# Performance work log

Measured on AMD Instinct MI355X. Metric: run time of the kernel, lower is better.

## Reference

```python
import jax, jax.numpy as jnp
import numpy as np

N_POINTS = 500000   # collocation points
N_TERMS = 64        # library terms
N_OUT = 4           # number of outputs / equations


def setup_inputs() -> dict:
    key = jax.random.key(0)
    k1, k2 = jax.random.split(key)
    thetas = jax.random.normal(k1, (N_POINTS, N_TERMS), dtype=jnp.float32)
    # n_out time derivatives packed as columns of a single [N, n_out] array
    time_derivs = jax.random.normal(k2, (N_POINTS, N_OUT), dtype=jnp.float32)
    return {"thetas": thetas, "time_derivs": time_derivs}


def reference(thetas, time_derivs):
    # sparsity masks are all-True at init, so apply_mask is identity and all
    # n_out least-squares problems share the same (full) library matrix.
    sparse_theta = thetas  # [N, n_terms]
    xtx = thetas.T @ thetas              # [n_terms, n_terms] (shared Gram)
    xty = thetas.T @ time_derivs         # [n_terms, n_out]
    # torch.inverse(X^T X) @ (X^T y), batched over outputs as columns
    coeffs = jnp.linalg.inv(xtx) @ xty   # [n_terms, n_out]
    return (sparse_theta, coeffs)
```

## Files before the change

### kernel.cpp

```cpp
#include <hip/hip_runtime.h>

#define N_ROWS   500000
#define N_TERMS  64
#define N_OUT    4
#define CHUNK_R  32
#define NCHUNK   (N_ROWS / CHUNK_R)
#define NB       512
#define WAVES_PB 8
#define WAVES_TOTAL (NB * WAVES_PB)
#define PART_STRIDE (N_TERMS * N_TERMS + N_TERMS * N_OUT)
#define CHUNKS   8
#define PER_CHUNK (NB / CHUNKS)
#define JACOBI_ITERS 20

typedef float f32x4   __attribute__((ext_vector_type(4)));
typedef short bf16x8  __attribute__((ext_vector_type(8)));

__device__ inline unsigned short f32_bf16(float f) {
  unsigned int u = __builtin_bit_cast(unsigned int, f);
  u += 0x7fffu + ((u >> 16) & 1u);
  return (unsigned short)(u >> 16);
}

__device__ inline bf16x8 frag_col(const float* __restrict__ Tf, int cswz, int k0) {
  bf16x8 r;
#pragma unroll
  for (int j = 0; j < 8; ++j)
    r[j] = (short)f32_bf16(Tf[(k0 + j) * 64 + cswz]);
  return r;
}

__global__ __launch_bounds__(512, 4) void k1_gram(const float* __restrict__ th,
                                                  const float* __restrict__ td,
                                                  float* __restrict__ out_copy,
                                                  float* __restrict__ part) {
  __shared__ float4 W4[WAVES_PB * 544];

  const int tid  = threadIdx.x;
  const int wv   = tid >> 6;
  const int lane = tid & 63;
  const int g    = lane >> 4;
  const int l15  = lane & 15;
  const int kg   = g * 8;
  const int szf  = (g & 1) << 4;

  float4* Wt = W4 + wv * 544;
  float4* Wy = Wt + 512;
  const float* Tf = (const float*)Wt;

  f32x4 c00 = {0.f,0.f,0.f,0.f}, c01 = c00, c02 = c00, c03 = c00;
  f32x4 c11 = c00, c12 = c00, c13 = c00, c22 = c00, c23 = c00, c33 = c00;
  float accY[4] = {0.f, 0.f, 0.f, 0.f};

  const float4* th4 = (const float4*)th;
  const float4* td4 = (const float4*)td;
  float4* out4 = (float4*)out_copy;

  for (int ch = blockIdx.x * WAVES_PB + wv; ch < NCHUNK; ch += WAVES_TOTAL) {
    const size_t r0 = (size_t)ch * CHUNK_R;
    const float4* src = th4 + r0 * 16;
    float4*       dst = out4 + r0 * 16;

    float4 cur[8];
#pragma unroll
    for (int j = 0; j < 8; ++j) cur[j] = src[j * 64 + lane];
    float4 yv = make_float4(0.f, 0.f, 0.f, 0.f);
    if (lane < 32) yv = td4[r0 + lane];

#pragma unroll
    for (int j = 0; j < 8; ++j) {
      dst[j * 64 + lane] = cur[j];
      const int fi  = j * 64 + lane;
      const int swz = ((fi >> 7) & 1) << 2;
      Wt[(fi & ~15) | ((fi & 15) ^ swz)] = cur[j];
    }
    if (lane < 32) Wy[lane] = yv;

    bf16x8 fr[4];
#pragma unroll
    for (int i = 0; i < 4; ++i)
      fr[i] = frag_col(Tf, (16 * i + l15) ^ szf, kg);

    c00 = __builtin_amdgcn_mfma_f32_16x16x32_bf16(fr[0], fr[0], c00, 0, 0, 0);
    c01 = __builtin_amdgcn_mfma_f32_16x16x32_bf16(fr[0], fr[1], c01, 0, 0, 0);
    c02 = __builtin_amdgcn_mfma_f32_16x16x32_bf16(fr[0], fr[2], c02, 0, 0, 0);
    c03 = __builtin_amdgcn_mfma_f32_16x16x32_bf16(fr[0], fr[3], c03, 0, 0, 0);
    c11 = __builtin_amdgcn_mfma_f32_16x16x32_bf16(fr[1], fr[1], c11, 0, 0, 0);
    c12 = __builtin_amdgcn_mfma_f32_16x16x32_bf16(fr[1], fr[2], c12, 0, 0, 0);
    c13 = __builtin_amdgcn_mfma_f32_16x16x32_bf16(fr[1], fr[3], c13, 0, 0, 0);
    c22 = __builtin_amdgcn_mfma_f32_16x16x32_bf16(fr[2], fr[2], c22, 0, 0, 0);
    c23 = __builtin_amdgcn_mfma_f32_16x16x32_bf16(fr[2], fr[3], c23, 0, 0, 0);
    c33 = __builtin_amdgcn_mfma_f32_16x16x32_bf16(fr[3], fr[3], c33, 0, 0, 0);

#pragma unroll
    for (int r = 0; r < CHUNK_R; ++r) {
      const int sz = ((r >> 3) & 1) << 4;
      const float  tv = Tf[r * 64 + (lane ^ sz)];
      const float4 yr = Wy[r];
      accY[0] += tv * yr.x;
      accY[1] += tv * yr.y;
      accY[2] += tv * yr.z;
      accY[3] += tv * yr.w;
    }
  }

  __syncthreads();
  float* red  = (float*)W4;
  float* yred = red + 64 * 65;

  for (int w = 0; w < WAVES_PB; ++w) {
    if (wv == w) {
      const bool first = (w == 0);
#define WR_TILE(A, B, C)                                                    \
  {                                                                         \
    _Pragma("unroll") for (int r = 0; r < 4; ++r) {                         \
      const int e = (16 * (A) + 4 * g + r) * 65 + 16 * (B) + l15;           \
      if (first) red[e] = (C)[r]; else red[e] += (C)[r];                    \
    }                                                                       \
  }
#define WR_TILE_T(A, B, C)                                                  \
  {                                                                         \
    _Pragma("unroll") for (int r = 0; r < 4; ++r) {                         \
      const int e = (16 * (B) + l15) * 65 + 16 * (A) + 4 * g + r;           \
      if (first) red[e] = (C)[r]; else red[e] += (C)[r];                    \
    }                                                                       \
  }
      WR_TILE(0, 0, c00);
      WR_TILE(0, 1, c01); WR_TILE_T(0, 1, c01);
      WR_TILE(0, 2, c02); WR_TILE_T(0, 2, c02);
      WR_TILE(0, 3, c03); WR_TILE_T(0, 3, c03);
      WR_TILE(1, 1, c11);
      WR_TILE(1, 2, c12); WR_TILE_T(1, 2, c12);
      WR_TILE(1, 3, c13); WR_TILE_T(1, 3, c13);
      WR_TILE(2, 2, c22);
      WR_TILE(2, 3, c23); WR_TILE_T(2, 3, c23);
      WR_TILE(3, 3, c33);
#undef WR_TILE
#undef WR_TILE_T
#pragma unroll
      for (int o = 0; o < 4; ++o) {
        const int e = lane * 4 + o;
        if (first) yred[e] = accY[o]; else yred[e] += accY[o];
      }
    }
    __syncthreads();
  }

  float* p = part + blockIdx.x * PART_STRIDE;
#pragma unroll
  for (int s = 0; s < 8; ++s) {
    const int e = s * 512 + tid;
    p[e] = red[(e >> 6) * 65 + (e & 63)];
  }
  if (tid < 256) p[4096 + tid] = yred[tid];
}

__global__ __launch_bounds__(256) void k2a_reduce(const float* __restrict__ part,
                                                  float* __restrict__ mid) {
  const int eblk = blockIdx.x % 17;
  const int bch  = blockIdx.x / 17;
  const int e = eblk * 256 + threadIdx.x;
  if (e >= PART_STRIDE) return;
  const float* base = part + (size_t)bch * PER_CHUNK * PART_STRIDE + e;
  float s = 0.f;
  for (int i = 0; i < PER_CHUNK; ++i) s += base[i * PART_STRIDE];
  mid[bch * PART_STRIDE + e] = s;
}

__global__ __launch_bounds__(256) void k3_solve(const float* __restrict__ mid,
                                                float* __restrict__ coef_out) {
  __shared__ float A[64 * 65];
  __shared__ float bX[64 * 4];
  __shared__ float X0[64 * 4];
  __shared__ float X1[64 * 4];
  const int tid = threadIdx.x;

#pragma unroll
  for (int s = 0; s < 17; ++s) {
    const int e = s * 256 + tid;
    if (e < PART_STRIDE) {
      float v = 0.f;
#pragma unroll
      for (int c = 0; c < CHUNKS; ++c) v += mid[c * PART_STRIDE + e];
      if (e < 4096) A[(e >> 6) * 65 + (e & 63)] = v;
      else          bX[e - 4096] = v;
    }
  }
  __syncthreads();

  const int i = tid >> 2;
  const int c = tid & 3;

  float arow[64];
#pragma unroll
  for (int j = 0; j < 64; ++j) arow[j] = A[i * 65 + j];

  const float dinv = 1.0f / A[i * 65 + i];
  const float b = bX[i * 4 + c];

  float x0 = b * dinv;
  X0[tid] = x0;
  __syncthreads();

  float xlast = x0;
  for (int it = 0; it < JACOBI_ITERS; ++it) {
    const float* Xr = (it & 1) ? X1 : X0;
    float*       Xw = (it & 1) ? X0 : X1;
    float s0 = 0.f, s1 = 0.f, s2 = 0.f, s3 = 0.f;
#pragma unroll
    for (int j = 0; j < 64; j += 4) {
      s0 += arow[j]     * Xr[(j)     * 4 + c];
      s1 += arow[j + 1] * Xr[(j + 1) * 4 + c];
      s2 += arow[j + 2] * Xr[(j + 2) * 4 + c];
      s3 += arow[j + 3] * Xr[(j + 3) * 4 + c];
    }
    const float s = (s0 + s1) + (s2 + s3);
    xlast = xlast + (b - s) * dinv;
    Xw[tid] = xlast;
    __syncthreads();
  }

  coef_out[tid] = xlast;
}

extern "C" void kernel_launch(void* const* d_in, const int* in_sizes, int n_in,
                              void* d_out, int out_size, void* d_ws, size_t ws_size,
                              hipStream_t stream) {
  const float* th = (const float*)d_in[0];
  const float* td = (const float*)d_in[1];
  float* out = (float*)d_out;
  float* ws  = (float*)d_ws;

  float* part = ws;
  float* mid  = ws + (size_t)NB * PART_STRIDE;

  hipLaunchKernelGGL(k1_gram, dim3(NB), dim3(512), 0, stream, th, td, out, part);
  hipLaunchKernelGGL(k2a_reduce, dim3(17 * CHUNKS), dim3(256), 0, stream, part, mid);
  hipLaunchKernelGGL(k3_solve, dim3(1), dim3(256), 0, stream, mid,
                     out + (size_t)N_ROWS * N_TERMS);
}
```

Before: 76.08 us.

## Split Gram kernel into copy waves and prefetching MFMA Gram waves

Result: slower. 159.2 us (+109.3%).

```diff
diff --git a/kernel.cpp b/kernel.cpp
--- a/kernel.cpp
+++ b/kernel.cpp
@@ -6,8 +6,8 @@
 #define CHUNK_R  32
 #define NCHUNK   (N_ROWS / CHUNK_R)
 #define NB       512
-#define WAVES_PB 8
-#define WAVES_TOTAL (NB * WAVES_PB)
+#define GRAM_WAVES_TOTAL (NB * 4)
+#define F4_TOTAL (N_ROWS * (N_TERMS / 4))
 #define PART_STRIDE (N_TERMS * N_TERMS + N_TERMS * N_OUT)
 #define CHUNKS   8
 #define PER_CHUNK (NB / CHUNKS)
@@ -34,7 +34,7 @@
                                                   const float* __restrict__ td,
                                                   float* __restrict__ out_copy,
                                                   float* __restrict__ part) {
-  __shared__ float4 W4[WAVES_PB * 544];
+  __shared__ float4 W4[4 * 544];
 
   const int tid  = threadIdx.x;
   const int wv   = tid >> 6;
@@ -44,63 +44,98 @@
   const int kg   = g * 8;
   const int szf  = (g & 1) << 4;
 
-  float4* Wt = W4 + wv * 544;
-  float4* Wy = Wt + 512;
-  const float* Tf = (const float*)Wt;
+  const float4* th4 = (const float4*)th;
+  const float4* td4 = (const float4*)td;
+  float4* out4 = (float4*)out_copy;
 
   f32x4 c00 = {0.f,0.f,0.f,0.f}, c01 = c00, c02 = c00, c03 = c00;
   f32x4 c11 = c00, c12 = c00, c13 = c00, c22 = c00, c23 = c00, c33 = c00;
   float accY[4] = {0.f, 0.f, 0.f, 0.f};
 
-  const float4* th4 = (const float4*)th;
-  const float4* td4 = (const float4*)td;
-  float4* out4 = (float4*)out_copy;
-
-  for (int ch = blockIdx.x * WAVES_PB + wv; ch < NCHUNK; ch += WAVES_TOTAL) {
-    const size_t r0 = (size_t)ch * CHUNK_R;
-    const float4* src = th4 + r0 * 16;
-    float4*       dst = out4 + r0 * 16;
-
-    float4 cur[8];
-#pragma unroll
-    for (int j = 0; j < 8; ++j) cur[j] = src[j * 64 + lane];
-    float4 yv = make_float4(0.f, 0.f, 0.f, 0.f);
-    if (lane < 32) yv = td4[r0 + lane];
-
-#pragma unroll
-    for (int j = 0; j < 8; ++j) {
-      dst[j * 64 + lane] = cur[j];
-      const int fi  = j * 64 + lane;
-      const int swz = ((fi >> 7) & 1) << 2;
-      Wt[(fi & ~15) | ((fi & 15) ^ swz)] = cur[j];
-    }
-    if (lane < 32) Wy[lane] = yv;
-
-    bf16x8 fr[4];
-#pragma unroll
-    for (int i = 0; i < 4; ++i)
-      fr[i] = frag_col(Tf, (16 * i + l15) ^ szf, kg);
-
-    c00 = __builtin_amdgcn_mfma_f32_16x16x32_bf16(fr[0], fr[0], c00, 0, 0, 0);
-    c01 = __builtin_amdgcn_mfma_f32_16x16x32_bf16(fr[0], fr[1], c01, 0, 0, 0);
-    c02 = __builtin_amdgcn_mfma_f32_16x16x32_bf16(fr[0], fr[2], c02, 0, 0, 0);
-    c03 = __builtin_amdgcn_mfma_f32_16x16x32_bf16(fr[0], fr[3], c03, 0, 0, 0);
-    c11 = __builtin_amdgcn_mfma_f32_16x16x32_bf16(fr[1], fr[1], c11, 0, 0, 0);
-    c12 = __builtin_amdgcn_mfma_f32_16x16x32_bf16(fr[1], fr[2], c12, 0, 0, 0);
-    c13 = __builtin_amdgcn_mfma_f32_16x16x32_bf16(fr[1], fr[3], c13, 0, 0, 0);
-    c22 = __builtin_amdgcn_mfma_f32_16x16x32_bf16(fr[2], fr[2], c22, 0, 0, 0);
-    c23 = __builtin_amdgcn_mfma_f32_16x16x32_bf16(fr[2], fr[3], c23, 0, 0, 0);
-    c33 = __builtin_amdgcn_mfma_f32_16x16x32_bf16(fr[3], fr[3], c33, 0, 0, 0);
-
-#pragma unroll
-    for (int r = 0; r < CHUNK_R; ++r) {
-      const int sz = ((r >> 3) & 1) << 4;
-      const float  tv = Tf[r * 64 + (lane ^ sz)];
-      const float4 yr = Wy[r];
-      accY[0] += tv * yr.x;
-      accY[1] += tv * yr.y;
-      accY[2] += tv * yr.z;
-      accY[3] += tv * yr.w;
+  if (wv >= 4) {
+    const int cwid = blockIdx.x * 4 + (wv - 4);
+#pragma unroll 1
+    for (int it = 0; it < 8; ++it) {
+      const int base = it * (2048 * 512) + cwid * 512 + lane;
+      float4 v[8];
+#pragma unroll
+      for (int u = 0; u < 8; ++u) {
+        const int idx = base + u * 64;
+        v[u] = (idx < F4_TOTAL) ? th4[idx] : make_float4(0.f, 0.f, 0.f, 0.f);
+      }
+#pragma unroll
+      for (int u = 0; u < 8; ++u) {
+        const int idx = base + u * 64;
+        if (idx < F4_TOTAL) out4[idx] = v[u];
+      }
+    }
+  } else {
+    float4* Wt = W4 + wv * 544;
+    float4* Wy = Wt + 512;
+    const float* Tf = (const float*)Wt;
+
+    int ch = blockIdx.x * 4 + wv;
+    float4 cur[8], yv;
+    if (ch < NCHUNK) {
+      const float4* src = th4 + (size_t)ch * 512;
+#pragma unroll
+      for (int j = 0; j < 8; ++j) cur[j] = src[j * 64 + lane];
+      yv = make_float4(0.f, 0.f, 0.f, 0.f);
+      if (lane < 32) yv = td4[(size_t)ch * CHUNK_R + lane];
+    }
+
+    while (ch < NCHUNK) {
+#pragma unroll
+      for (int j = 0; j < 8; ++j) {
+        const int fi  = j * 64 + lane;
+        const int swz = ((fi >> 7) & 1) << 2;
+        Wt[(fi & ~15) | ((fi & 15) ^ swz)] = cur[j];
+      }
+      if (lane < 32) Wy[lane] = yv;
+
+      const int chn = ch + GRAM_WAVES_TOTAL;
+      float4 nxt[8], ynxt;
+      if (chn < NCHUNK) {
+        const float4* srcn = th4 + (size_t)chn * 512;
+#pragma unroll
+        for (int j = 0; j < 8; ++j) nxt[j] = srcn[j * 64 + lane];
+        ynxt = make_float4(0.f, 0.f, 0.f, 0.f);
+        if (lane < 32) ynxt = td4[(size_t)chn * CHUNK_R + lane];
+      }
+
+      bf16x8 fr[4];
+#pragma unroll
+      for (int i = 0; i < 4; ++i)
+        fr[i] = frag_col(Tf, (16 * i + l15) ^ szf, kg);
+
+      c00 = __builtin_amdgcn_mfma_f32_16x16x32_bf16(fr[0], fr[0], c00, 0, 0, 0);
+      c01 = __builtin_amdgcn_mfma_f32_16x16x32_bf16(fr[0], fr[1], c01, 0, 0, 0);
+      c02 = __builtin_amdgcn_mfma_f32_16x16x32_bf16(fr[0], fr[2], c02, 0, 0, 0);
+      c03 = __builtin_amdgcn_mfma_f32_16x16x32_bf16(fr[0], fr[3], c03, 0, 0, 0);
+      c11 = __builtin_amdgcn_mfma_f32_16x16x32_bf16(fr[1], fr[1], c11, 0, 0, 0);
+      c12 = __builtin_amdgcn_mfma_f32_16x16x32_bf16(fr[1], fr[2], c12, 0, 0, 0);
+      c13 = __builtin_amdgcn_mfma_f32_16x16x32_bf16(fr[1], fr[3], c13, 0, 0, 0);
+      c22 = __builtin_amdgcn_mfma_f32_16x16x32_bf16(fr[2], fr[2], c22, 0, 0, 0);
+      c23 = __builtin_amdgcn_mfma_f32_16x16x32_bf16(fr[2], fr[3], c23, 0, 0, 0);
+      c33 = __builtin_amdgcn_mfma_f32_16x16x32_bf16(fr[3], fr[3], c33, 0, 0, 0);
+
+#pragma unroll
+      for (int r = 0; r < CHUNK_R; ++r) {
+        const int sz = ((r >> 3) & 1) << 4;
+        const float  tv = Tf[r * 64 + (lane ^ sz)];
+        const float4 yr = Wy[r];
+        accY[0] += tv * yr.x;
+        accY[1] += tv * yr.y;
+        accY[2] += tv * yr.z;
+        accY[3] += tv * yr.w;
+      }
+
+      ch = chn;
+      if (ch < NCHUNK) {
+#pragma unroll
+        for (int j = 0; j < 8; ++j) cur[j] = nxt[j];
+        yv = ynxt;
+      }
     }
   }
 
@@ -108,7 +143,7 @@
   float* red  = (float*)W4;
   float* yred = red + 64 * 65;
 
-  for (int w = 0; w < WAVES_PB; ++w) {
+  for (int w = 0; w < 4; ++w) {
     if (wv == w) {
       const bool first = (w == 0);
 #define WR_TILE(A, B, C)                                                    \
@@ -137,6 +172,8 @@
       WR_TILE(3, 3, c33);
 #undef WR_TILE
 #undef WR_TILE_T
+      if (g == 0) {
+      }
 #pragma unroll
       for (int o = 0; o < 4; ++o) {
         const int e = lane * 4 + o;
```
